# Kernel tuning notes

Hardware: AMD Instinct MI355X
Metric: run time of the kernel (lower is better)

The kernel has to match this reference:

```python
import jax, jax.numpy as jnp
import numpy as np

B, C, K, D = 16, 128, 128, 256
EPS = 1e-5  # torch BatchNorm1d default eps


def _bn(x, gamma, beta):
    # torch BatchNorm1d training-mode on (N, ch, L): normalize each channel over (N, L)
    mean = x.mean(axis=(0, 2), keepdims=True)
    var = x.var(axis=(0, 2), keepdims=True)  # biased, matches torch normalization
    return (x - mean) / jnp.sqrt(var + EPS) * gamma[None, :, None] + beta[None, :, None]


def setup_inputs() -> dict:
    key = jax.random.key(0)
    ks = jax.random.split(key, 6)
    q = jax.random.normal(ks[0], (B, C, D), jnp.float32)
    kc = jax.random.normal(ks[1], (B, K, D), jnp.float32)
    W0 = jax.random.normal(ks[2], (D, D), jnp.float32) / np.sqrt(D)
    W1 = jax.random.normal(ks[3], (D, D), jnp.float32) / np.sqrt(D)
    cmask = jax.random.randint(ks[4], (B, C), 0, 2, jnp.int32)
    kmask = jax.random.randint(ks[5], (B, K), 0, 2, jnp.int32)
    klen = jnp.maximum(kmask.sum(axis=1), 1).astype(jnp.int32)
    return {
        "query_candidates_repr": q,
        "key_candidates": kc,
        "W0": W0,
        "W1": W1,
        "bn0_gamma": jnp.ones((C,), jnp.float32),
        "bn0_beta": jnp.zeros((C,), jnp.float32),
        "bn1_gamma": jnp.ones((K,), jnp.float32),
        "bn1_beta": jnp.zeros((K,), jnp.float32),
        "query_candidate_mask": cmask,
        "key_candidate_mask": kmask,
        "key_candidate_len": klen,
    }


def reference(query_candidates_repr, key_candidates, W0, W1,
              bn0_gamma, bn0_beta, bn1_gamma, bn1_beta,
              query_candidate_mask, key_candidate_mask, key_candidate_len):
    # gated_attention branch (att_type != 'softmax'), activate = tanh
    g0 = _bn(query_candidates_repr @ W0.T, bn0_gamma, bn0_beta)  # (B,C,D)
    g1 = _bn(key_candidates @ W1.T, bn1_gamma, bn1_beta)          # (B,K,D)
    # (B,C,K,D) gate product
    attention_weight = jax.nn.sigmoid(g1)[:, None, :, :] * jax.nn.sigmoid(g0)[:, :, None, :]
    attention_res = key_candidates[:, None, :, :] * attention_weight  # (B,C,K,D)
    mask = (query_candidate_mask[:, :, None] * key_candidate_mask[:, None, :]).astype(jnp.float32)
    attention_res_masked = attention_res * mask[..., None]
    attention_vector = attention_res_masked.sum(axis=2) / key_candidate_len[:, None, None].astype(jnp.float32)
    output_res = jnp.tanh(attention_vector)  # (B,C,D)
    return output_res, attention_res_masked, attention_weight.mean(axis=-1)
```

## Files before the change

### kernel.cpp

```cpp
#include <hip/hip_runtime.h>


#define NB 16
#define NC 128
#define NK 128
#define ND 256

typedef float f4 __attribute__((ext_vector_type(4)));

__global__ __launch_bounds__(256) void k_gemm(const float* __restrict__ q,
                                              const float* __restrict__ kc,
                                              const float* __restrict__ W0,
                                              const float* __restrict__ W1,
                                              float* __restrict__ Y) {
    __shared__ float As[16][64];
    __shared__ float Bs[16][64];
    const int m0 = blockIdx.x * 64;
    const int d0 = blockIdx.y * 64;
    const int t  = threadIdx.x;
    const float* A = (m0 < 2048) ? (q + (size_t)m0 * ND) : (kc + (size_t)(m0 - 2048) * ND);
    const float* W = (m0 < 2048) ? W0 : W1;
    const int ml = t >> 2;
    const int jl = (t & 3) * 4;
    const int ty = t >> 4;
    const int tx = t & 15;

    float acc[4][4] = {};
    for (int j0 = 0; j0 < 256; j0 += 16) {
        float4 a = *(const float4*)(A + ml * ND + j0 + jl);
        float4 b = *(const float4*)(W + (d0 + ml) * ND + j0 + jl);
        As[jl + 0][ml] = a.x; As[jl + 1][ml] = a.y; As[jl + 2][ml] = a.z; As[jl + 3][ml] = a.w;
        Bs[jl + 0][ml] = b.x; Bs[jl + 1][ml] = b.y; Bs[jl + 2][ml] = b.z; Bs[jl + 3][ml] = b.w;
        __syncthreads();
#pragma unroll
        for (int jj = 0; jj < 16; ++jj) {
            float4 av = *(const float4*)&As[jj][ty * 4];
            float4 bv = *(const float4*)&Bs[jj][tx * 4];
            acc[0][0] += av.x * bv.x; acc[0][1] += av.x * bv.y; acc[0][2] += av.x * bv.z; acc[0][3] += av.x * bv.w;
            acc[1][0] += av.y * bv.x; acc[1][1] += av.y * bv.y; acc[1][2] += av.y * bv.z; acc[1][3] += av.y * bv.w;
            acc[2][0] += av.z * bv.x; acc[2][1] += av.z * bv.y; acc[2][2] += av.z * bv.z; acc[2][3] += av.z * bv.w;
            acc[3][0] += av.w * bv.x; acc[3][1] += av.w * bv.y; acc[3][2] += av.w * bv.z; acc[3][3] += av.w * bv.w;
        }
        __syncthreads();
    }
#pragma unroll
    for (int i = 0; i < 4; ++i) {
        float4 o = make_float4(acc[i][0], acc[i][1], acc[i][2], acc[i][3]);
        *(float4*)(Y + (size_t)(m0 + ty * 4 + i) * ND + d0 + tx * 4) = o;
    }
}

__global__ __launch_bounds__(256) void k_stats(const float* __restrict__ Y,
                                               const float* __restrict__ g0, const float* __restrict__ b0,
                                               const float* __restrict__ g1, const float* __restrict__ b1,
                                               float* __restrict__ sc, float* __restrict__ sh) {
    const int ch = blockIdx.x;
    const int t  = threadIdx.x;
    const int rbase = (ch < 128) ? ch : (2048 + (ch - 128));
    float s = 0.f, s2 = 0.f;
#pragma unroll
    for (int b = 0; b < NB; ++b) {
        float v = Y[(size_t)(rbase + b * 128) * ND + t];
        s += v; s2 += v * v;
    }
#pragma unroll
    for (int off = 32; off > 0; off >>= 1) {
        s  += __shfl_down(s,  off, 64);
        s2 += __shfl_down(s2, off, 64);
    }
    __shared__ float r1[4], r2[4];
    const int w = t >> 6;
    if ((t & 63) == 0) { r1[w] = s; r2[w] = s2; }
    __syncthreads();
    if (t == 0) {
        s  = r1[0] + r1[1] + r1[2] + r1[3];
        s2 = r2[0] + r2[1] + r2[2] + r2[3];
        float mean = s * (1.f / 4096.f);
        float var  = s2 * (1.f / 4096.f) - mean * mean;
        float rstd = rsqrtf(var + 1e-5f);
        float g  = (ch < 128) ? g0[ch] : g1[ch - 128];
        float be = (ch < 128) ? b0[ch] : b1[ch - 128];
        sc[ch] = g * rstd;
        sh[ch] = be - mean * g * rstd;
    }
}

__global__ __launch_bounds__(256) void k_apply(float* __restrict__ Y,
                                               const float* __restrict__ kc,
                                               const int* __restrict__ kmask,
                                               const float* __restrict__ sc, const float* __restrict__ sh,
                                               float* __restrict__ u) {
    const int m = blockIdx.x;
    const int t = threadIdx.x;
    const size_t idx = (size_t)m * ND + t;
    float x = Y[idx];
    const int ch = (m < 2048) ? (m & 127) : (128 + (m & 127));
    float g = x * sc[ch] + sh[ch];
    float v = 1.f / (1.f + __expf(-g));
    Y[idx] = v;
    if (m >= 2048) {
        const int mm = m - 2048;
        float uu = kmask[mm] ? (kc[(size_t)mm * ND + t] * v) : 0.f;
        u[(size_t)mm * ND + t] = uu;
    }
}

__global__ __launch_bounds__(256) void k_out2gemm(const float* __restrict__ Y,
                                                  float* __restrict__ out2) {
    __shared__ float As[16][64];
    __shared__ float Bs[16][64];
    const int b  = blockIdx.x;
    const int c0 = blockIdx.y * 64;
    const int k0 = blockIdx.z * 64;
    const int t  = threadIdx.x;
    const float* A = Y + (size_t)(b * 128 + c0) * ND;
    const float* W = Y + (size_t)(2048 + b * 128 + k0) * ND;
    const int ml = t >> 2;
    const int jl = (t & 3) * 4;
    const int ty = t >> 4;
    const int tx = t & 15;

    float acc[4][4] = {};
    for (int j0 = 0; j0 < 256; j0 += 16) {
        float4 a = *(const float4*)(A + ml * ND + j0 + jl);
        float4 w = *(const float4*)(W + ml * ND + j0 + jl);
        As[jl + 0][ml] = a.x; As[jl + 1][ml] = a.y; As[jl + 2][ml] = a.z; As[jl + 3][ml] = a.w;
        Bs[jl + 0][ml] = w.x; Bs[jl + 1][ml] = w.y; Bs[jl + 2][ml] = w.z; Bs[jl + 3][ml] = w.w;
        __syncthreads();
#pragma unroll
        for (int jj = 0; jj < 16; ++jj) {
            float4 av = *(const float4*)&As[jj][ty * 4];
            float4 bv = *(const float4*)&Bs[jj][tx * 4];
            acc[0][0] += av.x * bv.x; acc[0][1] += av.x * bv.y; acc[0][2] += av.x * bv.z; acc[0][3] += av.x * bv.w;
            acc[1][0] += av.y * bv.x; acc[1][1] += av.y * bv.y; acc[1][2] += av.y * bv.z; acc[1][3] += av.y * bv.w;
            acc[2][0] += av.z * bv.x; acc[2][1] += av.z * bv.y; acc[2][2] += av.z * bv.z; acc[2][3] += av.z * bv.w;
            acc[3][0] += av.w * bv.x; acc[3][1] += av.w * bv.y; acc[3][2] += av.w * bv.z; acc[3][3] += av.w * bv.w;
        }
        __syncthreads();
    }
    float* ob = out2 + (size_t)b * 128 * 128;
#pragma unroll
    for (int i = 0; i < 4; ++i) {
        float4 o = make_float4(acc[i][0] * (1.f / 256.f), acc[i][1] * (1.f / 256.f),
                               acc[i][2] * (1.f / 256.f), acc[i][3] * (1.f / 256.f));
        *(float4*)(ob + (size_t)(c0 + ty * 4 + i) * 128 + k0 + tx * 4) = o;
    }
}

__global__ __launch_bounds__(256) void k_big2(const float* __restrict__ Y,
                                              const float* __restrict__ u,
                                              const int* __restrict__ cmask,
                                              const int* __restrict__ klen,
                                              float* __restrict__ out0,
                                              float* __restrict__ out1) {
    const int bc = blockIdx.x;
    const int b  = bc >> 7;
    const int t  = threadIdx.x;
    const int f  = t & 63;
    const int g  = t >> 6;

    float4 s0v = *(const float4*)(Y + (size_t)bc * ND + f * 4);
    const bool cm = cmask[bc] != 0;
    float4 v0 = cm ? s0v : make_float4(0.f, 0.f, 0.f, 0.f);

    const float* ub = u + (size_t)b * 128 * ND;
    f4* o1 = (f4*)(out1 + (size_t)bc * 128 * ND);

    float tx_ = 0.f, ty_ = 0.f, tz_ = 0.f, tw_ = 0.f;
#pragma unroll 8
    for (int k0 = 0; k0 < 32; ++k0) {
        const int k = k0 * 4 + g;
        float4 uv = *(const float4*)(ub + (size_t)k * ND + f * 4);
        f4 ov = { v0.x * uv.x, v0.y * uv.y, v0.z * uv.z, v0.w * uv.w };
        __builtin_nontemporal_store(ov, o1 + (size_t)k * 64 + f);
        tx_ += uv.x; ty_ += uv.y; tz_ += uv.z; tw_ += uv.w;
    }

    __shared__ float tl[4][256];
    *(float4*)&tl[g][f * 4] = make_float4(tx_, ty_, tz_, tw_);
    __syncthreads();
    if (g == 0) {
        float4 t0 = *(const float4*)&tl[0][f * 4];
        float4 t1 = *(const float4*)&tl[1][f * 4];
        float4 t2 = *(const float4*)&tl[2][f * 4];
        float4 t3 = *(const float4*)&tl[3][f * 4];
        const float inv = 1.f / (float)klen[b];
        float ax = tanhf(v0.x * (t0.x + t1.x + t2.x + t3.x) * inv);
        float ay = tanhf(v0.y * (t0.y + t1.y + t2.y + t3.y) * inv);
        float az = tanhf(v0.z * (t0.z + t1.z + t2.z + t3.z) * inv);
        float aw = tanhf(v0.w * (t0.w + t1.w + t2.w + t3.w) * inv);
        *(float4*)(out0 + (size_t)bc * ND + f * 4) = make_float4(ax, ay, az, aw);
    }
}

extern "C" void kernel_launch(void* const* d_in, const int* in_sizes, int n_in,
                              void* d_out, int out_size, void* d_ws, size_t ws_size,
                              hipStream_t stream) {
    const float* q     = (const float*)d_in[0];
    const float* kc    = (const float*)d_in[1];
    const float* W0    = (const float*)d_in[2];
    const float* W1    = (const float*)d_in[3];
    const float* g0    = (const float*)d_in[4];
    const float* b0    = (const float*)d_in[5];
    const float* g1    = (const float*)d_in[6];
    const float* b1    = (const float*)d_in[7];
    const int*   cmask = (const int*)d_in[8];
    const int*   kmask = (const int*)d_in[9];
    const int*   klen  = (const int*)d_in[10];

    float* ws = (float*)d_ws;
    float* Y  = ws;
    float* u  = ws + 1048576;
    float* sc = ws + 1572864;
    float* sh = ws + 1573120;

    float* o    = (float*)d_out;
    float* out0 = o;
    float* out1 = o + 524288;
    float* out2 = o + 67633152;

    k_gemm<<<dim3(64, 4), 256, 0, stream>>>(q, kc, W0, W1, Y);
    k_stats<<<256, 256, 0, stream>>>(Y, g0, b0, g1, b1, sc, sh);
    k_apply<<<4096, 256, 0, stream>>>(Y, kc, kmask, sc, sh, u);
    k_out2gemm<<<dim3(16, 2, 2), 256, 0, stream>>>(Y, out2);
    k_big2<<<2048, 256, 0, stream>>>(Y, u, cmask, klen, out0, out1);
}
```

Before: 329.8 us.

## Split big output kernel into out0 reduction kernel and k-major out1 writer

After: 336.8 us. +2.1%, slower.

```diff
diff --git a/kernel.cpp b/kernel.cpp
--- a/kernel.cpp
+++ b/kernel.cpp
@@ -147,49 +147,62 @@
     }
 }
 
-__global__ __launch_bounds__(256) void k_big2(const float* __restrict__ Y,
+__global__ __launch_bounds__(256) void k_out1(const float* __restrict__ Y,
                                               const float* __restrict__ u,
                                               const int* __restrict__ cmask,
-                                              const int* __restrict__ klen,
-                                              float* __restrict__ out0,
                                               float* __restrict__ out1) {
-    const int bc = blockIdx.x;
-    const int b  = bc >> 7;
+    const int b  = blockIdx.x;
+    const int kt = blockIdx.y;
     const int t  = threadIdx.x;
     const int f  = t & 63;
     const int g  = t >> 6;
-
-    float4 s0v = *(const float4*)(Y + (size_t)bc * ND + f * 4);
-    const bool cm = cmask[bc] != 0;
-    float4 v0 = cm ? s0v : make_float4(0.f, 0.f, 0.f, 0.f);
+    const int k  = kt * 4 + g;
+
+    float4 uv = *(const float4*)(u + ((size_t)(b * 128 + k)) * ND + f * 4);
+    const float* s0b = Y + (size_t)b * 128 * ND;
+    const int* cmb = cmask + b * 128;
+
+#pragma unroll 4
+    for (int c = 0; c < 128; ++c) {
+        float4 s0v = *(const float4*)(s0b + (size_t)c * ND + f * 4);
+        const float sel = cmb[c] ? 1.f : 0.f;
+        f4 ov = { sel * s0v.x * uv.x, sel * s0v.y * uv.y,
+                  sel * s0v.z * uv.z, sel * s0v.w * uv.w };
+        __builtin_nontemporal_store(ov,
+            (f4*)(out1 + (((size_t)(b * 128 + c)) * 128 + k) * ND) + f);
+    }
+}
+
+__global__ __launch_bounds__(256) void k_tvec_out0(const float* __restrict__ Y,
+                                                   const float* __restrict__ u,
+                                                   const int* __restrict__ cmask,
+                                                   const int* __restrict__ klen,
+                                                   float* __restrict__ out0) {
+    const int b  = blockIdx.x;
+    const int dc = blockIdx.y * 64;
+    const int t  = threadIdx.x;
+    const int f  = t & 63;
+    const int g  = t >> 6;
+    const int d  = dc + f;
 
     const float* ub = u + (size_t)b * 128 * ND;
-    f4* o1 = (f4*)(out1 + (size_t)bc * 128 * ND);
-
-    float tx_ = 0.f, ty_ = 0.f, tz_ = 0.f, tw_ = 0.f;
+    float s = 0.f;
 #pragma unroll 8
-    for (int k0 = 0; k0 < 32; ++k0) {
-        const int k = k0 * 4 + g;
-        float4 uv = *(const float4*)(ub + (size_t)k * ND + f * 4);
-        f4 ov = { v0.x * uv.x, v0.y * uv.y, v0.z * uv.z, v0.w * uv.w };
-        __builtin_nontemporal_store(ov, o1 + (size_t)k * 64 + f);
-        tx_ += uv.x; ty_ += uv.y; tz_ += uv.z; tw_ += uv.w;
-    }
-
-    __shared__ float tl[4][256];
-    *(float4*)&tl[g][f * 4] = make_float4(tx_, ty_, tz_, tw_);
+    for (int k0 = 0; k0 < 32; ++k0) s += ub[(size_t)(k0 * 4 + g) * ND + d];
+
+    __shared__ float red[4][64];
+    red[g][f] = s;
     __syncthreads();
-    if (g == 0) {
-        float4 t0 = *(const float4*)&tl[0][f * 4];
-        float4 t1 = *(const float4*)&tl[1][f * 4];
-        float4 t2 = *(const float4*)&tl[2][f * 4];
-        float4 t3 = *(const float4*)&tl[3][f * 4];
-        const float inv = 1.f / (float)klen[b];
-        float ax = tanhf(v0.x * (t0.x + t1.x + t2.x + t3.x) * inv);
-        float ay = tanhf(v0.y * (t0.y + t1.y + t2.y + t3.y) * inv);
-        float az = tanhf(v0.z * (t0.z + t1.z + t2.z + t3.z) * inv);
-        float aw = tanhf(v0.w * (t0.w + t1.w + t2.w + t3.w) * inv);
-        *(float4*)(out0 + (size_t)bc * ND + f * 4) = make_float4(ax, ay, az, aw);
+    const float tval = (red[0][f] + red[1][f] + red[2][f] + red[3][f]) / (float)klen[b];
+
+    const float* s0b = Y + (size_t)b * 128 * ND;
+    const int* cmb = cmask + b * 128;
+#pragma unroll 4
+    for (int c0 = 0; c0 < 32; ++c0) {
+        const int c = c0 * 4 + g;
+        float s0 = s0b[(size_t)c * ND + d];
+        float v0 = cmb[c] ? s0 : 0.f;
+        out0[((size_t)(b * 128 + c)) * ND + d] = tanhf(v0 * tval);
     }
 }
 
@@ -223,5 +236,6 @@
     k_stats<<<256, 256, 0, stream>>>(Y, g0, b0, g1, b1, sc, sh);
     k_apply<<<4096, 256, 0, stream>>>(Y, kc, kmask, sc, sh, u);
     k_out2gemm<<<dim3(16, 2, 2), 256, 0, stream>>>(Y, out2);
-    k_big2<<<2048, 256, 0, stream>>>(Y, u, cmask, klen, out0, out1);
-}
+    k_tvec_out0<<<dim3(16, 4), 256, 0, stream>>>(Y, u, cmask, klen, out0);
+    k_out1<<<dim3(16, 32), 256, 0, stream>>>(Y, u, cmask, out1);
+}
```
